# Performance work log

Measured on AMD Instinct MI355X. Metric: run time of the kernel, lower is better.

## Reference

```python
import math
import jax, jax.numpy as jnp
import numpy as np

IN_FEATURES = 4096
OUT_FEATURES = 4096
BLOCK_SIZE = 256
N_TOKENS = 8192


def _butterfly_layout(out_blocks, in_blocks, butterfly_size):
    # sum of log2(n) butterfly factors with all-ones 2x2 twiddles:
    # block (o, i) is active iff o == i or o == i ^ 2^k for some factor k
    log_n = int(math.log2(butterfly_size))
    idx = np.arange(butterfly_size)
    layout = np.zeros((butterfly_size, butterfly_size), dtype=bool)
    layout[idx, idx] = True
    for k in range(log_n):
        layout[idx ^ (1 << k), idx] = True
    if out_blocks > butterfly_size:
        layout = np.tile(layout, (out_blocks // butterfly_size, 1))
    if in_blocks > butterfly_size:
        layout = np.tile(layout, (1, in_blocks // butterfly_size))
    return layout


def _flat_indices(layout):
    # For each output block, flat indices into [num_in_blocks * active_blocks_per_input]
    # selecting which per-input weight blocks are summed (embedding_bag mode='sum').
    num_out, num_in = layout.shape
    abpi = int(layout.sum(0)[0])
    abpo = int(layout.sum(1)[0])
    rank = np.cumsum(layout, axis=0) - 1  # rank of output o among active outputs of input i
    o_idx, i_idx = np.nonzero(layout)     # row-major -> grouped by output block
    flat = i_idx * abpi + rank[o_idx, i_idx]
    return flat.reshape(num_out, abpo).astype(np.int32), abpi


def setup_inputs() -> dict:
    key = jax.random.key(0)
    k1, k2 = jax.random.split(key)
    in_blocks = IN_FEATURES // BLOCK_SIZE
    out_blocks = OUT_FEATURES // BLOCK_SIZE
    butterfly_size = min(IN_FEATURES, OUT_FEATURES) // BLOCK_SIZE  # 16
    layout = _butterfly_layout(out_blocks, in_blocks, butterfly_size)
    flat_idx, abpi = _flat_indices(layout)  # abpi = log2(16)+1 = 5
    std = math.sqrt(2.0 / (5 * min(IN_FEATURES, OUT_FEATURES)))
    weight = jax.random.normal(k1, (IN_FEATURES, abpi, BLOCK_SIZE), dtype=jnp.float32) * std
    x = jax.random.normal(k2, (N_TOKENS, IN_FEATURES), dtype=jnp.float32)
    return {"x": x, "weight": weight, "flat_indices": jnp.asarray(flat_idx)}


def reference(x, weight, flat_indices):
    # x: [B, in_features]; weight: [in_features, abpi, block_size]
    in_features, abpi, bs = weight.shape
    num_in = in_features // bs
    B = x.shape[0]
    xb = x.reshape(B, num_in, bs)                  # [B, g, k]
    w = weight.reshape(num_in, bs, abpi, bs)       # [g, k, a, o]
    # per-input-block partial output blocks: [g, a, B, o]
    blocks = jnp.einsum('bgk,gkao->gabo', xb, w)
    blocks = blocks.reshape(num_in * abpi, B, bs)
    # gather + sum active blocks per output block (embedding_bag mode='sum')
    out_blocks = blocks[flat_indices].sum(axis=1)  # [num_out_blocks, B, bs]
    out = jnp.transpose(out_blocks, (1, 0, 2)).reshape(B, -1)  # [B, out_features]
    return out
```

## Files before the change

kernel.cpp:

```cpp
#include <hip/hip_runtime.h>
#include <stdint.h>

#define N_TOK 8192
#define IN_F 4096
#define OUT_F 4096
#define BS 256
#define ABPI 5
#define NFLAT 80

typedef __attribute__((ext_vector_type(8))) short short8;
typedef __attribute__((ext_vector_type(4))) float floatx4;
typedef __attribute__((ext_vector_type(4))) unsigned short ushort4v;
typedef __attribute__((ext_vector_type(8))) unsigned short ushort8v;

__device__ __forceinline__ unsigned short f2bf(float f) {
  union { float f; unsigned int u; } v; v.f = f;
  unsigned int r = v.u + 0x7FFFu + ((v.u >> 16) & 1u);
  return (unsigned short)(r >> 16);
}

__device__ __forceinline__ void async16(const void* g, void* l) {
  __builtin_amdgcn_global_load_lds((const __attribute__((address_space(1))) void*)g,
                                   (__attribute__((address_space(3))) void*)l, 16, 0, 0);
}

__global__ void cvt_x_kernel(const float4* __restrict__ x, ushort8v* __restrict__ xb) {
  int idx = blockIdx.x * 256 + threadIdx.x;
  float4 a = x[idx * 2], b = x[idx * 2 + 1];
  ushort8v o;
  o[0] = f2bf(a.x); o[1] = f2bf(a.y); o[2] = f2bf(a.z); o[3] = f2bf(a.w);
  o[4] = f2bf(b.x); o[5] = f2bf(b.y); o[6] = f2bf(b.z); o[7] = f2bf(b.w);
  xb[idx] = o;
}

__global__ void cvt_w_kernel(const float* __restrict__ w, unsigned short* __restrict__ wt) {
  __shared__ unsigned short tile[64][68];
  int b = blockIdx.x;
  int fi = b >> 4;
  int t  = b & 15;
  int k0 = (t >> 2) * 64, o0 = (t & 3) * 64;
  int g = fi / ABPI, a = fi % ABPI;
  int tid = threadIdx.x;
  int tr = tid >> 4, tc = tid & 15;
  #pragma unroll
  for (int i = 0; i < 4; ++i) {
    int k = k0 + i * 16 + tr;
    const float* src = w + (size_t)(g * 256 + k) * (ABPI * BS) + a * BS + o0 + tc * 4;
    float4 v = *(const float4*)src;
    tile[tc * 4 + 0][i * 16 + tr] = f2bf(v.x);
    tile[tc * 4 + 1][i * 16 + tr] = f2bf(v.y);
    tile[tc * 4 + 2][i * 16 + tr] = f2bf(v.z);
    tile[tc * 4 + 3][i * 16 + tr] = f2bf(v.w);
  }
  __syncthreads();
  #pragma unroll
  for (int i = 0; i < 4; ++i) {
    int o = i * 16 + tr;
    unsigned short* dst = wt + (size_t)fi * (BS * BS) + (size_t)(o0 + o) * BS + k0 + tc * 4;
    *(ushort4v*)dst = *(const ushort4v*)&tile[o][tc * 4];
  }
}


#define BM 256
#define BN 256
#define BK 64
#define ABYTES 32768
#define BUFBYTES 65536
#define SMEM_TOTAL 131072

__device__ __forceinline__ void ld_half_A(const char* p, int c0, int c1, short8 (&af)[4][2]) {
  #pragma unroll
  for (int mt = 0; mt < 4; ++mt) {
    const char* q = p + mt * 2048;
    af[mt][0] = *(const short8*)(q + c0);
    af[mt][1] = *(const short8*)(q + c1);
  }
}

__device__ __forceinline__ void ld_pair_B(const char* p, int c0, int c1, short8 (&bf)[2][2]) {
  #pragma unroll
  for (int nt = 0; nt < 2; ++nt) {
    const char* q = p + nt * 2048;
    bf[nt][0] = *(const short8*)(q + c0);
    bf[nt][1] = *(const short8*)(q + c1);
  }
}

__device__ __forceinline__ void mma16(const short8 (&af)[4][2], const short8 (&bf)[2][2],
                                      floatx4 (&acc)[8][4], int mb, int nb) {
  #pragma unroll
  for (int mt = 0; mt < 4; ++mt)
    #pragma unroll
    for (int nt = 0; nt < 2; ++nt) {
      acc[mb + mt][nb + nt] =
          __builtin_amdgcn_mfma_f32_16x16x32_bf16(af[mt][0], bf[nt][0], acc[mb + mt][nb + nt], 0, 0, 0);
      acc[mb + mt][nb + nt] =
          __builtin_amdgcn_mfma_f32_16x16x32_bf16(af[mt][1], bf[nt][1], acc[mb + mt][nb + nt], 0, 0, 0);
    }
}

#define PH_OPEN                                            \
  __builtin_amdgcn_s_barrier();                            \
  asm volatile("s_waitcnt lgkmcnt(0)" ::: "memory");       \
  __builtin_amdgcn_sched_barrier(0);                       \
  __builtin_amdgcn_s_setprio(1)

#define KTILE(tt, Ab, Bb, Asd, Bsd, DOSTAGE, LAST)                              \
  do {                                                                          \
    int uA = 0, uB = 0;                                                         \
    if (DOSTAGE) { const int u = (tt) + 1, su = u >> 2, ku = (u & 3) * 64;      \
                   uA = gcol[su] + ku; uB = wbase[su] + ku; }                   \
                                                \
    ld_half_A((Ab) + rAb, c0, c1, af);                                          \
    ld_pair_B((Bb) + rBb, c0, c1, bf01);                                        \
    if (DOSTAGE) { async16(pA0 + uA, (Asd)         + tid16);                    \
                   async16(pA2 + uA, (Asd) + 16384 + tid16);                    \
                   async16(pB0 + uB, (Bsd)         + tid16);                    \
                   async16(pB1 + uB, (Bsd) +  8192 + tid16); }                  \
    PH_OPEN; mma16(af, bf01, acc, 0, 0);                                        \
    __builtin_amdgcn_s_setprio(0);                                              \
    __builtin_amdgcn_s_barrier();                                               \
                                                \
    ld_pair_B((Bb) + rBb + 4096, c0, c1, bf23);                                 \
    if (DOSTAGE) { async16(pB2 + uB, (Bsd) + 16384 + tid16);                    \
                   async16(pB3 + uB, (Bsd) + 24576 + tid16); }                  \
    PH_OPEN; mma16(af, bf23, acc, 0, 2);                                        \
    __builtin_amdgcn_s_setprio(0);                                              \
    if (DOSTAGE)   { asm volatile("s_waitcnt vmcnt(6)" ::: "memory");           \
                     __builtin_amdgcn_sched_barrier(0); }                       \
    else if (LAST) { asm volatile("s_waitcnt vmcnt(0)" ::: "memory");           \
                     __builtin_amdgcn_sched_barrier(0); }                       \
    __builtin_amdgcn_s_barrier();                                               \
                                                \
    ld_half_A((Ab) + rAb + 8192, c0, c1, af);                                   \
    if (DOSTAGE) { async16(pA1 + uA, (Asd) +  8192 + tid16);                    \
                   async16(pA3 + uA, (Asd) + 24576 + tid16); }                  \
    PH_OPEN; mma16(af, bf23, acc, 4, 2);                                        \
    __builtin_amdgcn_s_setprio(0);                                              \
    __builtin_amdgcn_s_barrier();                                               \
                          \
    __builtin_amdgcn_s_setprio(1);                                              \
    mma16(af, bf01, acc, 4, 0);                                                 \
    __builtin_amdgcn_s_setprio(0);                                              \
    if (DOSTAGE) { asm volatile("s_waitcnt vmcnt(2)" ::: "memory");             \
                   __builtin_amdgcn_sched_barrier(0); }                         \
    __builtin_amdgcn_s_barrier();                                               \
  } while (0)

__global__ __launch_bounds__(512, 2)
void bfly_gemm(const unsigned short* __restrict__ xb,
               const unsigned short* __restrict__ wt,
               const int* __restrict__ fidx,
               float* __restrict__ out)
{
  extern __shared__ __align__(16) char smem[];
  char* const b0A = smem;
  char* const b0B = b0A + ABYTES;
  char* const b1A = smem + BUFBYTES;
  char* const b1B = b1A + ABYTES;

  const int tid = threadIdx.x;
  const int bx  = blockIdx.x;
  const int swz = (bx & 7) * 64 + (bx >> 3);
  const int ob  = swz >> 5;
  const int mt0 = swz & 31;
  const int m0  = mt0 * BM;
  const int n0g = ob * 256;

  int wbase[ABPI], gcol[ABPI];
  #pragma unroll
  for (int s = 0; s < ABPI; ++s) {
    int fi = __builtin_amdgcn_readfirstlane(fidx[ob * ABPI + s]);
    wbase[s] = fi * (BS * BS);
    gcol[s]  = (fi / ABPI) * BS;
  }

  const int sr = tid >> 3;
  const int sc = tid & 7;
  const int lc = sc ^ (sr & 7);
  const int tid16 = tid * 16;
  const unsigned short* pA0 = xb + (size_t)(m0 +   0 + sr) * IN_F + lc * 8;
  const unsigned short* pA1 = xb + (size_t)(m0 +  64 + sr) * IN_F + lc * 8;
  const unsigned short* pA2 = xb + (size_t)(m0 + 128 + sr) * IN_F + lc * 8;
  const unsigned short* pA3 = xb + (size_t)(m0 + 192 + sr) * IN_F + lc * 8;
  const unsigned short* pB0 = wt + (  0 + sr) * BS + lc * 8;
  const unsigned short* pB1 = wt + ( 64 + sr) * BS + lc * 8;
  const unsigned short* pB2 = wt + (128 + sr) * BS + lc * 8;
  const unsigned short* pB3 = wt + (192 + sr) * BS + lc * 8;

  const int lane = tid & 63;
  const int wv   = tid >> 6;
  const int wm   = (wv >> 2) * 128;
  const int wn   = (wv & 3) * 64;
  const int lrow = lane & 15;
  const int quad = lane >> 4;
  const int rAb  = (wm + lrow) * 128;
  const int rBb  = (wn + lrow) * 128;
  const int c0   = ((quad)     ^ (lrow & 7)) * 16;
  const int c1   = ((quad + 4) ^ (lrow & 7)) * 16;

  short8 af[4][2], bf01[2][2], bf23[2][2];
  floatx4 acc[8][4] = {};

  {
    const int uA0 = gcol[0], uB0 = wbase[0];
    async16(pA0 + uA0, b0A         + tid16);
    async16(pA1 + uA0, b0A +  8192 + tid16);
    async16(pA2 + uA0, b0A + 16384 + tid16);
    async16(pA3 + uA0, b0A + 24576 + tid16);
    async16(pB0 + uB0, b0B         + tid16);
    async16(pB1 + uB0, b0B +  8192 + tid16);
    async16(pB2 + uB0, b0B + 16384 + tid16);
    async16(pB3 + uB0, b0B + 24576 + tid16);
    asm volatile("s_waitcnt vmcnt(0)" ::: "memory");
    __builtin_amdgcn_sched_barrier(0);
    __builtin_amdgcn_s_barrier();
  }

  #pragma unroll 1
  for (int j = 0; j < 9; ++j) {
    const int t = j * 2;
    KTILE(t,     b0A, b0B, b1A, b1B, true, false);
    KTILE(t + 1, b1A, b1B, b0A, b0B, true, false);
  }
  KTILE(18, b0A, b0B, b1A, b1B, true, false);
  KTILE(19, b1A, b1B, b0A, b0B, false, true);

  #pragma unroll
  for (int m = 0; m < 8; ++m) {
    const int row = m0 + wm + (m >> 2) * 64 + (m & 3) * 16 + quad * 4;
    #pragma unroll
    for (int n = 0; n < 4; ++n) {
      const int col = n0g + wn + n * 16 + lrow;
      float* po = out + (size_t)row * OUT_F + col;
      #pragma unroll
      for (int r = 0; r < 4; ++r)
        po[(size_t)r * OUT_F] = acc[m][n][r];
    }
  }
}

extern "C" void kernel_launch(void* const* d_in, const int* in_sizes, int n_in,
                              void* d_out, int out_size, void* d_ws, size_t ws_size,
                              hipStream_t stream) {
  const float* x  = (const float*)d_in[0];
  const float* w  = (const float*)d_in[1];
  const int* fidx = (const int*)d_in[2];
  float* out = (float*)d_out;

  unsigned short* xb = (unsigned short*)d_ws;
  unsigned short* wt = xb + (size_t)N_TOK * IN_F;

  static int smem_set = 0;
  if (!smem_set) {
    hipFuncSetAttribute((const void*)bfly_gemm,
                        hipFuncAttributeMaxDynamicSharedMemorySize, SMEM_TOTAL);
    smem_set = 1;
  }

  cvt_x_kernel<<<(N_TOK * IN_F) / (8 * 256), 256, 0, stream>>>((const float4*)x, (ushort8v*)xb);
  cvt_w_kernel<<<NFLAT * 16, 256, 0, stream>>>(w, wt);
  bfly_gemm<<<16 * 32, 512, SMEM_TOTAL, stream>>>(xb, wt, fidx, out);
}
```

Baseline: 323.6 us.

## Restructure K-tile pipeline with fewer barriers and rework x conversion grid-stride loop

The GEMM K-tile macro drops the four-phase barrier schedule: all eight async global-to-LDS loads for the next stage are issued up front, LDS fragment reads are batched with partial lgkmcnt waits, and a single vmcnt(0) plus one barrier closes each tile. This aims to cut per-tile barrier and synchronisation overhead, but it gives up interleaving loads with MFMA phases and waits for every prefetch at tile end. Separately, the x fp32-to-bf16 conversion now launches a fixed 2048-block grid, and each thread loops 16 times over one float4 at a time with a grid-sized stride, instead of handling two float4s per thread in one pass.

```diff
diff --git a/kernel.cpp b/kernel.cpp
--- a/kernel.cpp
+++ b/kernel.cpp
@@ -11,7 +11,6 @@
 typedef __attribute__((ext_vector_type(8))) short short8;
 typedef __attribute__((ext_vector_type(4))) float floatx4;
 typedef __attribute__((ext_vector_type(4))) unsigned short ushort4v;
-typedef __attribute__((ext_vector_type(8))) unsigned short ushort8v;
 
 __device__ __forceinline__ unsigned short f2bf(float f) {
   union { float f; unsigned int u; } v; v.f = f;
@@ -24,13 +23,16 @@
                                    (__attribute__((address_space(3))) void*)l, 16, 0, 0);
 }
 
-__global__ void cvt_x_kernel(const float4* __restrict__ x, ushort8v* __restrict__ xb) {
+__global__ void cvt_x_kernel(const float4* __restrict__ x, ushort4v* __restrict__ xb) {
   int idx = blockIdx.x * 256 + threadIdx.x;
-  float4 a = x[idx * 2], b = x[idx * 2 + 1];
-  ushort8v o;
-  o[0] = f2bf(a.x); o[1] = f2bf(a.y); o[2] = f2bf(a.z); o[3] = f2bf(a.w);
-  o[4] = f2bf(b.x); o[5] = f2bf(b.y); o[6] = f2bf(b.z); o[7] = f2bf(b.w);
-  xb[idx] = o;
+  const int stride = 2048 * 256;
+  #pragma unroll
+  for (int i = 0; i < 16; ++i, idx += stride) {
+    float4 a = x[idx];
+    ushort4v o;
+    o[0] = f2bf(a.x); o[1] = f2bf(a.y); o[2] = f2bf(a.z); o[3] = f2bf(a.w);
+    xb[idx] = o;
+  }
 }
 
 __global__ void cvt_w_kernel(const float* __restrict__ w, unsigned short* __restrict__ wt) {
@@ -100,52 +102,48 @@
     }
 }
 
-#define PH_OPEN                                            \
-  __builtin_amdgcn_s_barrier();                            \
-  asm volatile("s_waitcnt lgkmcnt(0)" ::: "memory");       \
-  __builtin_amdgcn_sched_barrier(0);                       \
-  __builtin_amdgcn_s_setprio(1)
-
 #define KTILE(tt, Ab, Bb, Asd, Bsd, DOSTAGE, LAST)                              \
   do {                                                                          \
-    int uA = 0, uB = 0;                                                         \
-    if (DOSTAGE) { const int u = (tt) + 1, su = u >> 2, ku = (u & 3) * 64;      \
-                   uA = gcol[su] + ku; uB = wbase[su] + ku; }                   \
-                                                \
-    ld_half_A((Ab) + rAb, c0, c1, af);                                          \
-    ld_pair_B((Bb) + rBb, c0, c1, bf01);                                        \
-    if (DOSTAGE) { async16(pA0 + uA, (Asd)         + tid16);                    \
-                   async16(pA2 + uA, (Asd) + 16384 + tid16);                    \
-                   async16(pB0 + uB, (Bsd)         + tid16);                    \
-                   async16(pB1 + uB, (Bsd) +  8192 + tid16); }                  \
-    PH_OPEN; mma16(af, bf01, acc, 0, 0);                                        \
+    if (DOSTAGE) {                                                              \
+      const int u = (tt) + 1, su = u >> 2, ku = (u & 3) * 64;                   \
+      const int uA = gcol[su] + ku, uB = wbase[su] + ku;                        \
+      async16(pA0 + uA, (Asd)         + tid16);                                 \
+      async16(pA1 + uA, (Asd) +  8192 + tid16);                                 \
+      async16(pA2 + uA, (Asd) + 16384 + tid16);                                 \
+      async16(pA3 + uA, (Asd) + 24576 + tid16);                                 \
+      async16(pB0 + uB, (Bsd)         + tid16);                                 \
+      async16(pB1 + uB, (Bsd) +  8192 + tid16);                                 \
+      async16(pB2 + uB, (Bsd) + 16384 + tid16);                                 \
+      async16(pB3 + uB, (Bsd) + 24576 + tid16);                                 \
+    }                                                                           \
+    ld_half_A((Ab) + rAb, c0, c1, af);                      \
+    ld_pair_B((Bb) + rBb, c0, c1, bf01);                                 \
+    ld_pair_B((Bb) + rBb + 4096, c0, c1, bf23);                          \
+    asm volatile("s_waitcnt lgkmcnt(4)" ::: "memory");    \
+    __builtin_amdgcn_sched_barrier(0);                                          \
+    __builtin_amdgcn_s_setprio(1);                                              \
+    mma16(af, bf01, acc, 0, 0);                    \
     __builtin_amdgcn_s_setprio(0);                                              \
-    __builtin_amdgcn_s_barrier();                                               \
-                                                \
-    ld_pair_B((Bb) + rBb + 4096, c0, c1, bf23);                                 \
-    if (DOSTAGE) { async16(pB2 + uB, (Bsd) + 16384 + tid16);                    \
-                   async16(pB3 + uB, (Bsd) + 24576 + tid16); }                  \
-    PH_OPEN; mma16(af, bf23, acc, 0, 2);                                        \
+    asm volatile("s_waitcnt lgkmcnt(0)" ::: "memory");                          \
+    __builtin_amdgcn_sched_barrier(0);                                          \
+    __builtin_amdgcn_s_setprio(1);                                              \
+    mma16(af, bf23, acc, 0, 2);                                         \
     __builtin_amdgcn_s_setprio(0);                                              \
-    if (DOSTAGE)   { asm volatile("s_waitcnt vmcnt(6)" ::: "memory");           \
-                     __builtin_amdgcn_sched_barrier(0); }                       \
-    else if (LAST) { asm volatile("s_waitcnt vmcnt(0)" ::: "memory");           \
-                     __builtin_amdgcn_sched_barrier(0); }                       \
-    __builtin_amdgcn_s_barrier();                                               \
-                                                \
-    ld_half_A((Ab) + rAb + 8192, c0, c1, af);                                   \
-    if (DOSTAGE) { async16(pA1 + uA, (Asd) +  8192 + tid16);                    \
-                   async16(pA3 + uA, (Asd) + 24576 + tid16); }                  \
-    PH_OPEN; mma16(af, bf23, acc, 4, 2);                                        \
+    __builtin_amdgcn_sched_barrier(0);            \
+    ld_half_A((Ab) + rAb + 8192, c0, c1, af);             \
+    asm volatile("s_waitcnt lgkmcnt(0)" ::: "memory");                          \
+    __builtin_amdgcn_sched_barrier(0);                                          \
+    __builtin_amdgcn_s_setprio(1);                                              \
+    mma16(af, bf23, acc, 4, 2);                                         \
+    mma16(af, bf01, acc, 4, 0);                        \
     __builtin_amdgcn_s_setprio(0);                                              \
-    __builtin_amdgcn_s_barrier();                                               \
-                          \
-    __builtin_amdgcn_s_setprio(1);                                              \
-    mma16(af, bf01, acc, 4, 0);                                                 \
-    __builtin_amdgcn_s_setprio(0);                                              \
-    if (DOSTAGE) { asm volatile("s_waitcnt vmcnt(2)" ::: "memory");             \
-                   __builtin_amdgcn_sched_barrier(0); }                         \
-    __builtin_amdgcn_s_barrier();                                               \
+    if (DOSTAGE) {                                                              \
+      asm volatile("s_waitcnt vmcnt(0)" ::: "memory");    \
+      __builtin_amdgcn_sched_barrier(0);                                        \
+      __builtin_amdgcn_s_barrier();                  \
+    } else if (!(LAST)) {                                                       \
+      __builtin_amdgcn_s_barrier();                                             \
+    }                                                                           \
   } while (0)
 
 __global__ __launch_bounds__(512, 2)
@@ -259,7 +257,7 @@
     smem_set = 1;
   }
 
-  cvt_x_kernel<<<(N_TOK * IN_F) / (8 * 256), 256, 0, stream>>>((const float4*)x, (ushort8v*)xb);
+  cvt_x_kernel<<<2048, 256, 0, stream>>>((const float4*)x, (ushort4v*)xb);
   cvt_w_kernel<<<NFLAT * 16, 256, 0, stream>>>(w, wt);
   bfly_gemm<<<16 * 32, 512, SMEM_TOTAL, stream>>>(xb, wt, fidx, out);
 }
```

Result: no change. 327.9 us (+1.3%).
